# Optimization experiments

Hardware: AMD Instinct MI355X
Metric: run time of the kernel (lower is better)

The kernel has to match this reference:

```python
import jax, jax.numpy as jnp
import numpy as np

NBINS = 256  # skimage threshold_otsu default
SMOOTH = 1.0


def _otsu_threshold(x):
    """Otsu threshold of a flat float array, skimage-style 256-bin histogram."""
    x = x.reshape(-1)
    xmin = x.min()
    xmax = x.max()
    span = xmax - xmin
    scale = jnp.where(span > 0, NBINS / span, 0.0)
    idx = jnp.clip(((x - xmin) * scale).astype(jnp.int32), 0, NBINS - 1)
    hist = jnp.zeros(NBINS, dtype=x.dtype).at[idx].add(1.0)
    centers = xmin + (jnp.arange(NBINS, dtype=x.dtype) + 0.5) * (span / NBINS)
    # class weights and means (first bin always contains min, last contains max,
    # so the cumulative sums used below are strictly positive)
    w1 = jnp.cumsum(hist)
    w2 = jnp.cumsum(hist[::-1])
    m1 = jnp.cumsum(hist * centers) / w1
    m2 = (jnp.cumsum((hist * centers)[::-1]) / w2)[::-1]
    w2 = w2[::-1]
    var12 = w1[:-1] * w2[1:] * (m1[:-1] - m2[1:]) ** 2  # inter-class variance
    return centers[jnp.argmax(var12)]


def setup_inputs() -> dict:
    key = jax.random.key(0)
    k1, k2 = jax.random.split(key)
    B, C, H, W = 64, 1, 512, 512
    output = jax.random.normal(k1, (B, C, H, W), dtype=jnp.float32)
    target = (jax.random.uniform(k2, (B, C, H, W)) > 0.5).astype(jnp.float32)
    return {"output": output, "target": target}


def reference(output, target):
    probs = jax.nn.sigmoid(output)                    # [B,C,H,W]
    thresh = jax.vmap(_otsu_threshold)(probs)         # per-sample Otsu, [B]
    binary = (probs > thresh[:, None, None, None]).astype(probs.dtype)
    intersection = (binary * target).sum(axis=(-1, -2))          # [B,C]
    union = (binary + target).sum(axis=(-1, -2)) - intersection  # [B,C]
    iou = (intersection + SMOOTH) / (union + SMOOTH)
    return iou.mean()  # reduction='mean'
```

## Files before the change

### kernel.cpp

```cpp
#include <hip/hip_runtime.h>
#include <cstdint>

static constexpr int BATCH = 64;
static constexpr int NPB   = 512 * 512;
static constexpr int NFB   = 2048;
static constexpr int PBLK  = 16;
static constexpr int ELB   = NPB / PBLK;

static constexpr int W_BMIN = 0;
static constexpr int W_BMAX = 4096;
static constexpr int W_PART = 8192;

__device__ __forceinline__ float sigmoidf(float v) {
  if (v >= 0.0f) return 1.0f / (1.0f + expf(-v));
  float e = expf(v);
  return e / (1.0f + e);
}
__device__ __forceinline__ float fsig(float v) {
  return __builtin_amdgcn_rcpf(1.0f + __expf(-v));
}

__global__ __launch_bounds__(256) void k_pass(const float* __restrict__ x,
                                              const float* __restrict__ tg,
                                              uint32_t* __restrict__ ws,
                                              float* __restrict__ out) {
  constexpr int ITER = ELB / 4 / 256;
  __shared__ uint32_t h[2 * NFB];
  const int t = threadIdx.x;
  const int g = blockIdx.x;
  if (g == 0 && t == 0) out[0] = 0.0f;
#pragma unroll
  for (int j = 0; j < 4; ++j)
    reinterpret_cast<uint4*>(h)[t + j * 256] = uint4{0u, 0u, 0u, 0u};
  __syncthreads();

  const int b = g >> 4;
  const int blk = g & 15;
  const size_t base = (size_t)b * NPB + (size_t)blk * ELB;
  const float4* px = reinterpret_cast<const float4*>(x + base);
  const float4* pt = reinterpret_cast<const float4*>(tg + base);
  const uint32_t woff = (uint32_t)(t >> 7) << 11;

  float mn = INFINITY, mx = -INFINITY;
#pragma unroll 4
  for (int i = 0; i < ITER; ++i) {
    float4 v = px[i * 256 + t];
    float4 w = pt[i * 256 + t];
    mn = fminf(mn, fminf(fminf(v.x, v.y), fminf(v.z, v.w)));
    mx = fmaxf(mx, fmaxf(fmaxf(v.x, v.y), fmaxf(v.z, v.w)));
#define PUT(a, c) { int idx = (int)(fsig(a) * 2048.0f);                        \
                    idx = idx > 2047 ? 2047 : idx;                             \
                    const uint32_t val = ((c) > 0.5f) ? 0x10001u : 1u;         \
                    (void)__hip_atomic_fetch_add(&h[woff + idx], val,          \
                        __ATOMIC_RELAXED, __HIP_MEMORY_SCOPE_WORKGROUP); }
    PUT(v.x, w.x) PUT(v.y, w.y) PUT(v.z, w.z) PUT(v.w, w.w)
#undef PUT
  }
  for (int off = 32; off; off >>= 1) {
    mn = fminf(mn, __shfl_down(mn, off));
    mx = fmaxf(mx, __shfl_down(mx, off));
  }
  if ((t & 63) == 0) {
    float* wsf = reinterpret_cast<float*>(ws);
    wsf[W_BMIN + g * 4 + (t >> 6)] = mn;
    wsf[W_BMAX + g * 4 + (t >> 6)] = mx;
  }
  __syncthreads();
  uint32_t* gp = ws + W_PART + (size_t)g * NFB;
#pragma unroll
  for (int j = 0; j < 8; ++j) {
    const int w = t + j * 256;
    gp[w] = h[w] + h[w + 2048];
  }
}

__global__ __launch_bounds__(256) void k_finalize(uint32_t* __restrict__ ws,
                                                  float* __restrict__ out) {
  __shared__ uint32_t tot[NFB];
  __shared__ uint32_t pos[NFB];
  __shared__ uint32_t h256[256];
  __shared__ uint32_t w1s[256];
  __shared__ float s1s[256];
  __shared__ float vv[256];
  __shared__ int vi[256];
  __shared__ unsigned long long redL[256];
  __shared__ float sPmin, sScale, sBinw;
  const int b = blockIdx.x;
  const int t = threadIdx.x;
  const float* wsf = reinterpret_cast<const float*>(ws);

#pragma unroll
  for (int j = 0; j < 8; ++j) {
    const int w = t + j * 256;
    uint32_t at = 0, ap = 0;
#pragma unroll
    for (int p = 0; p < PBLK; ++p) {
      const uint32_t v = ws[W_PART + (size_t)(b * PBLK + p) * NFB + w];
      at += v & 0xFFFFu;
      ap += v >> 16;
    }
    tot[w] = at;
    pos[w] = ap;
  }
  h256[t] = 0u;
  if (t < 64) {
    float mnv = INFINITY, mxv = -INFINITY;
    for (int i = t; i < PBLK * 4; i += 64) {
      mnv = fminf(mnv, wsf[W_BMIN + b * PBLK * 4 + i]);
      mxv = fmaxf(mxv, wsf[W_BMAX + b * PBLK * 4 + i]);
    }
    for (int off = 32; off; off >>= 1) {
      mnv = fminf(mnv, __shfl_down(mnv, off));
      mxv = fmaxf(mxv, __shfl_down(mxv, off));
    }
    if (t == 0) {
      const float pmin = sigmoidf(mnv);
      const float pmax = sigmoidf(mxv);
      const float span = pmax - pmin;
      sPmin = pmin;
      sScale = (span > 0.0f) ? (512.0f / span) : 0.0f;
      sBinw = span * (1.0f / 256.0f);
    }
  }
  __syncthreads();
  const float pmin = sPmin, scale = sScale, binw = sBinw;

#define CIDX(k) ({ const float rep = ((float)(k) + 0.5f) * (1.0f / 2048.0f);  \
                   int ci = (int)((rep - pmin) * scale);                      \
                   ci = ci < 0 ? 0 : (ci > 511 ? 511 : ci); ci; })
#pragma unroll
  for (int j = 0; j < 8; ++j) {
    const int k = t + j * 256;
    if (tot[k]) atomicAdd(&h256[CIDX(k) >> 1], tot[k]);
  }
  __syncthreads();

  const uint32_t hk = h256[t];
  const float ck = pmin + ((float)t + 0.5f) * binw;
  w1s[t] = hk;
  s1s[t] = (float)hk * ck;
  for (int off = 1; off < 256; off <<= 1) {
    __syncthreads();
    uint32_t wp = (t >= off) ? w1s[t - off] : 0u;
    float    sp = (t >= off) ? s1s[t - off] : 0.0f;
    __syncthreads();
    w1s[t] += wp; s1s[t] += sp;
  }
  __syncthreads();
  const uint32_t totW = w1s[255];
  const float totS = s1s[255];
  float v = -INFINITY;
  if (t < 255 && w1s[t] > 0u && totW > w1s[t]) {
    const float w1f = (float)w1s[t];
    const float w2f = (float)(totW - w1s[t]);
    const float m1 = s1s[t] / w1f;
    const float m2 = (totS - s1s[t]) / w2f;
    const float d = m1 - m2;
    v = (w1f * w2f) * (d * d);
  }
  vv[t] = v; vi[t] = t;
  for (int s = 128; s; s >>= 1) {
    __syncthreads();
    if (t < s) {
      const float vb = vv[t + s]; const int ib = vi[t + s];
      if (vb > vv[t] || (vb == vv[t] && ib < vi[t])) { vv[t] = vb; vi[t] = ib; }
    }
  }
  __syncthreads();
  const int J = 2 * vi[0] + 1;

  uint32_t nb_p = 0, ni_p = 0, nt_p = 0;
#pragma unroll
  for (int j = 0; j < 8; ++j) {
    const int k = t + j * 256;
    const uint32_t ct = tot[k], cp = pos[k];
    nt_p += cp;
    if (CIDX(k) >= J) { nb_p += ct; ni_p += cp; }
  }
#undef CIDX
  redL[t] = (unsigned long long)nb_p | ((unsigned long long)ni_p << 20) | ((unsigned long long)nt_p << 40);
  for (int s = 128; s; s >>= 1) {
    __syncthreads();
    if (t < s) redL[t] += redL[t + s];
  }
  __syncthreads();
  if (t == 0) {
    const unsigned long long P = redL[0];
    const float nb = (float)(uint32_t)(P & 0xFFFFFu);
    const float ni = (float)(uint32_t)((P >> 20) & 0xFFFFFu);
    const float nt = (float)(uint32_t)((P >> 40) & 0xFFFFFu);
    const float uni = nb + nt - ni;
    const float iou = (ni + 1.0f) / (uni + 1.0f);
    atomicAdd(out, iou * (1.0f / 64.0f));
  }
}

extern "C" void kernel_launch(void* const* d_in, const int* in_sizes, int n_in,
                              void* d_out, int out_size, void* d_ws, size_t ws_size,
                              hipStream_t stream) {
  const float* x  = (const float*)d_in[0];
  const float* tg = (const float*)d_in[1];
  uint32_t* ws = (uint32_t*)d_ws;
  float* out = (float*)d_out;

  hipLaunchKernelGGL(k_pass,     dim3(BATCH * PBLK), dim3(256), 0, stream, x, tg, ws, out);
  hipLaunchKernelGGL(k_finalize, dim3(BATCH),        dim3(256), 0, stream, ws, out);
}
```

Measured before the change: 35.05 us.

## Fuse histogram and finalize into one kernel using last-block-done counters

```diff
diff --git a/kernel.cpp b/kernel.cpp
--- a/kernel.cpp
+++ b/kernel.cpp
@@ -4,12 +4,15 @@
 static constexpr int BATCH = 64;
 static constexpr int NPB   = 512 * 512;
 static constexpr int NFB   = 2048;
-static constexpr int PBLK  = 16;
+static constexpr int PBLK  = 8;
 static constexpr int ELB   = NPB / PBLK;
 
 static constexpr int W_BMIN = 0;
-static constexpr int W_BMAX = 4096;
-static constexpr int W_PART = 8192;
+static constexpr int W_BMAX = 512;
+static constexpr int W_T1   = 1024;
+static constexpr int W_T3   = 3072;
+static constexpr int W_IOU  = 3104;
+static constexpr int W_PART = 4096;
 
 __device__ __forceinline__ float sigmoidf(float v) {
   if (v >= 0.0f) return 1.0f / (1.0f + expf(-v));
@@ -19,23 +22,46 @@
 __device__ __forceinline__ float fsig(float v) {
   return __builtin_amdgcn_rcpf(1.0f + __expf(-v));
 }
-
-__global__ __launch_bounds__(256) void k_pass(const float* __restrict__ x,
+__device__ __forceinline__ uint32_t llc_load(const uint32_t* p) {
+  return __hip_atomic_load(p, __ATOMIC_RELAXED, __HIP_MEMORY_SCOPE_SYSTEM);
+}
+__device__ __forceinline__ float llc_loadf(const float* p) {
+  return __hip_atomic_load(p, __ATOMIC_RELAXED, __HIP_MEMORY_SCOPE_SYSTEM);
+}
+__device__ __forceinline__ void llc_store(uint32_t* p, uint32_t v) {
+  __hip_atomic_store(p, v, __ATOMIC_RELAXED, __HIP_MEMORY_SCOPE_SYSTEM);
+}
+__device__ __forceinline__ void llc_storef(float* p, float v) {
+  __hip_atomic_store(p, v, __ATOMIC_RELAXED, __HIP_MEMORY_SCOPE_SYSTEM);
+}
+
+__global__ __launch_bounds__(256) void k_init(uint32_t* __restrict__ ws) {
+  for (int i = threadIdx.x; i < 2080; i += 256) ws[W_T1 + i] = 0u;
+}
+
+__global__ __launch_bounds__(256) void k_main(const float* __restrict__ x,
                                               const float* __restrict__ tg,
                                               uint32_t* __restrict__ ws,
                                               float* __restrict__ out) {
-  constexpr int ITER = ELB / 4 / 256;
-  __shared__ uint32_t h[2 * NFB];
-  const int t = threadIdx.x;
-  const int g = blockIdx.x;
-  if (g == 0 && t == 0) out[0] = 0.0f;
-#pragma unroll
-  for (int j = 0; j < 4; ++j)
-    reinterpret_cast<uint4*>(h)[t + j * 256] = uint4{0u, 0u, 0u, 0u};
-  __syncthreads();
-
-  const int b = g >> 4;
-  const int blk = g & 15;
+  __shared__ uint32_t pool[4096];
+  __shared__ uint32_t h256[256];
+  __shared__ uint32_t scanA[256];
+  __shared__ float    scanB[256];
+  __shared__ float    scanC[256];
+  __shared__ int      scanD[256];
+  __shared__ unsigned long long redL[256];
+  __shared__ float smn[4], smx[4];
+  __shared__ int sFlag, sLast;
+  __shared__ float sPmin, sScale, sBinw;
+  const int t = threadIdx.x, g = blockIdx.x;
+  const int b = g >> 3, blk = g & 7;
+  float* wsf = reinterpret_cast<float*>(ws);
+
+#pragma unroll
+  for (int q = 0; q < 4; ++q)
+    reinterpret_cast<uint4*>(pool)[t + q * 256] = uint4{0u, 0u, 0u, 0u};
+  __syncthreads();
+
   const size_t base = (size_t)b * NPB + (size_t)blk * ELB;
   const float4* px = reinterpret_cast<const float4*>(x + base);
   const float4* pt = reinterpret_cast<const float4*>(tg + base);
@@ -43,7 +69,7 @@
 
   float mn = INFINITY, mx = -INFINITY;
 #pragma unroll 4
-  for (int i = 0; i < ITER; ++i) {
+  for (int i = 0; i < 32; ++i) {
     float4 v = px[i * 256 + t];
     float4 w = pt[i * 256 + t];
     mn = fminf(mn, fminf(fminf(v.x, v.y), fminf(v.z, v.w)));
@@ -51,7 +77,7 @@
 #define PUT(a, c) { int idx = (int)(fsig(a) * 2048.0f);                        \
                     idx = idx > 2047 ? 2047 : idx;                             \
                     const uint32_t val = ((c) > 0.5f) ? 0x10001u : 1u;         \
-                    (void)__hip_atomic_fetch_add(&h[woff + idx], val,          \
+                    (void)__hip_atomic_fetch_add(&pool[woff + idx], val,       \
                         __ATOMIC_RELAXED, __HIP_MEMORY_SCOPE_WORKGROUP); }
     PUT(v.x, w.x) PUT(v.y, w.y) PUT(v.z, w.z) PUT(v.w, w.w)
 #undef PUT
@@ -60,125 +86,120 @@
     mn = fminf(mn, __shfl_down(mn, off));
     mx = fmaxf(mx, __shfl_down(mx, off));
   }
-  if ((t & 63) == 0) {
-    float* wsf = reinterpret_cast<float*>(ws);
-    wsf[W_BMIN + g * 4 + (t >> 6)] = mn;
-    wsf[W_BMAX + g * 4 + (t >> 6)] = mx;
-  }
-  __syncthreads();
+  if ((t & 63) == 0) { smn[t >> 6] = mn; smx[t >> 6] = mx; }
+  __syncthreads();
+  if (t == 0) {
+    mn = fminf(fminf(smn[0], smn[1]), fminf(smn[2], smn[3]));
+    mx = fmaxf(fmaxf(smx[0], smx[1]), fmaxf(smx[2], smx[3]));
+    llc_storef(&wsf[W_BMIN + g], mn);
+    llc_storef(&wsf[W_BMAX + g], mx);
+  }
   uint32_t* gp = ws + W_PART + (size_t)g * NFB;
 #pragma unroll
-  for (int j = 0; j < 8; ++j) {
-    const int w = t + j * 256;
-    gp[w] = h[w] + h[w + 2048];
-  }
-}
-
-__global__ __launch_bounds__(256) void k_finalize(uint32_t* __restrict__ ws,
-                                                  float* __restrict__ out) {
-  __shared__ uint32_t tot[NFB];
-  __shared__ uint32_t pos[NFB];
-  __shared__ uint32_t h256[256];
-  __shared__ uint32_t w1s[256];
-  __shared__ float s1s[256];
-  __shared__ float vv[256];
-  __shared__ int vi[256];
-  __shared__ unsigned long long redL[256];
-  __shared__ float sPmin, sScale, sBinw;
-  const int b = blockIdx.x;
-  const int t = threadIdx.x;
-  const float* wsf = reinterpret_cast<const float*>(ws);
-
-#pragma unroll
-  for (int j = 0; j < 8; ++j) {
-    const int w = t + j * 256;
+  for (int q = 0; q < 8; ++q) {
+    const int w_ = t + q * 256;
+    llc_store(&gp[w_], pool[w_] + pool[w_ + 2048]);
+  }
+  __syncthreads();
+  if (t == 0) {
+    asm volatile("s_waitcnt vmcnt(0)" ::: "memory");
+    sFlag = (atomicAdd(&ws[W_T1 + b * 32], 1u) == PBLK - 1);
+  }
+  __syncthreads();
+  if (!sFlag) return;
+
+#pragma unroll
+  for (int q = 0; q < 8; ++q) {
+    const int k = t + q * 256;
     uint32_t at = 0, ap = 0;
 #pragma unroll
     for (int p = 0; p < PBLK; ++p) {
-      const uint32_t v = ws[W_PART + (size_t)(b * PBLK + p) * NFB + w];
+      const uint32_t v = llc_load(&ws[W_PART + (size_t)(b * 8 + p) * NFB + k]);
       at += v & 0xFFFFu;
       ap += v >> 16;
     }
-    tot[w] = at;
-    pos[w] = ap;
+    scanA[0] = scanA[0];
+    pool[k] = at | 0u;
+    redL[t] = 0ull;
+    pool[k + 2048] = ap;
   }
   h256[t] = 0u;
-  if (t < 64) {
-    float mnv = INFINITY, mxv = -INFINITY;
-    for (int i = t; i < PBLK * 4; i += 64) {
-      mnv = fminf(mnv, wsf[W_BMIN + b * PBLK * 4 + i]);
-      mxv = fmaxf(mxv, wsf[W_BMAX + b * PBLK * 4 + i]);
+  float mnv = (t < 8) ? llc_loadf(&wsf[W_BMIN + b * 8 + t]) : INFINITY;
+  float mxv = (t < 8) ? llc_loadf(&wsf[W_BMAX + b * 8 + t]) : -INFINITY;
+  for (int off = 4; off; off >>= 1) {
+    mnv = fminf(mnv, __shfl_down(mnv, off));
+    mxv = fmaxf(mxv, __shfl_down(mxv, off));
+  }
+  if (t == 0) {
+    const float pmin = sigmoidf(mnv);
+    const float pmax = sigmoidf(mxv);
+    const float span = pmax - pmin;
+    sPmin = pmin;
+    sScale = (span > 0.0f) ? (512.0f / span) : -1.0f;
+    sBinw = span * (1.0f / 256.0f);
+  }
+  __syncthreads();
+  const float pmin = sPmin, scale = sScale, binw = sBinw;
+  const bool degen = (scale < 0.0f);
+#define CIDX(k) ({ const float rep = ((float)(k) + 0.5f) * (1.0f / 2048.0f);  \
+                   int ci_ = (int)((rep - pmin) * scale);                     \
+                   ci_ = ci_ < 0 ? 0 : (ci_ > 511 ? 511 : ci_); ci_; })
+  if (!degen) {
+#pragma unroll
+    for (int q = 0; q < 8; ++q) {
+      const int k = t + q * 256;
+      const uint32_t ct = pool[k];
+      if (ct) atomicAdd(&h256[CIDX(k) >> 1], ct);
     }
-    for (int off = 32; off; off >>= 1) {
-      mnv = fminf(mnv, __shfl_down(mnv, off));
-      mxv = fmaxf(mxv, __shfl_down(mxv, off));
-    }
-    if (t == 0) {
-      const float pmin = sigmoidf(mnv);
-      const float pmax = sigmoidf(mxv);
-      const float span = pmax - pmin;
-      sPmin = pmin;
-      sScale = (span > 0.0f) ? (512.0f / span) : 0.0f;
-      sBinw = span * (1.0f / 256.0f);
-    }
-  }
-  __syncthreads();
-  const float pmin = sPmin, scale = sScale, binw = sBinw;
-
-#define CIDX(k) ({ const float rep = ((float)(k) + 0.5f) * (1.0f / 2048.0f);  \
-                   int ci = (int)((rep - pmin) * scale);                      \
-                   ci = ci < 0 ? 0 : (ci > 511 ? 511 : ci); ci; })
-#pragma unroll
-  for (int j = 0; j < 8; ++j) {
-    const int k = t + j * 256;
-    if (tot[k]) atomicAdd(&h256[CIDX(k) >> 1], tot[k]);
-  }
-  __syncthreads();
-
+  }
+  __syncthreads();
   const uint32_t hk = h256[t];
   const float ck = pmin + ((float)t + 0.5f) * binw;
-  w1s[t] = hk;
-  s1s[t] = (float)hk * ck;
+  scanA[t] = hk;
+  scanB[t] = (float)hk * ck;
   for (int off = 1; off < 256; off <<= 1) {
     __syncthreads();
-    uint32_t wp = (t >= off) ? w1s[t - off] : 0u;
-    float    sp = (t >= off) ? s1s[t - off] : 0.0f;
-    __syncthreads();
-    w1s[t] += wp; s1s[t] += sp;
-  }
-  __syncthreads();
-  const uint32_t totW = w1s[255];
-  const float totS = s1s[255];
-  float v = -INFINITY;
-  if (t < 255 && w1s[t] > 0u && totW > w1s[t]) {
-    const float w1f = (float)w1s[t];
-    const float w2f = (float)(totW - w1s[t]);
-    const float m1 = s1s[t] / w1f;
-    const float m2 = (totS - s1s[t]) / w2f;
+    uint32_t wp = (t >= off) ? scanA[t - off] : 0u;
+    float    sp = (t >= off) ? scanB[t - off] : 0.0f;
+    __syncthreads();
+    scanA[t] += wp; scanB[t] += sp;
+  }
+  __syncthreads();
+  const uint32_t totW = scanA[255];
+  const float totS = scanB[255];
+  float vv = -INFINITY;
+  if (t < 255 && scanA[t] > 0u && totW > scanA[t]) {
+    const float w1f = (float)scanA[t];
+    const float w2f = (float)(totW - scanA[t]);
+    const float m1 = scanB[t] / w1f;
+    const float m2 = (totS - scanB[t]) / w2f;
     const float d = m1 - m2;
-    v = (w1f * w2f) * (d * d);
-  }
-  vv[t] = v; vi[t] = t;
+    vv = (w1f * w2f) * (d * d);
+  }
+  scanC[t] = vv; scanD[t] = t;
   for (int s = 128; s; s >>= 1) {
     __syncthreads();
     if (t < s) {
-      const float vb = vv[t + s]; const int ib = vi[t + s];
-      if (vb > vv[t] || (vb == vv[t] && ib < vi[t])) { vv[t] = vb; vi[t] = ib; }
+      const float vb = scanC[t + s]; const int ib = scanD[t + s];
+      if (vb > scanC[t] || (vb == scanC[t] && ib < scanD[t])) {
+        scanC[t] = vb; scanD[t] = ib;
+      }
     }
   }
   __syncthreads();
-  const int J = 2 * vi[0] + 1;
-
-  uint32_t nb_p = 0, ni_p = 0, nt_p = 0;
-#pragma unroll
-  for (int j = 0; j < 8; ++j) {
-    const int k = t + j * 256;
-    const uint32_t ct = tot[k], cp = pos[k];
-    nt_p += cp;
-    if (CIDX(k) >= J) { nb_p += ct; ni_p += cp; }
+  const int Jh = degen ? (1 << 20) : (2 * scanD[0] + 1);
+  uint32_t nb = 0, ni = 0, nt = 0;
+#pragma unroll
+  for (int q = 0; q < 8; ++q) {
+    const int k = t + q * 256;
+    const uint32_t ct = pool[k], cp = pool[k + 2048];
+    nt += cp;
+    const int ci = degen ? 0 : CIDX(k);
+    if (ci >= Jh) { nb += ct; ni += cp; }
   }
 #undef CIDX
-  redL[t] = (unsigned long long)nb_p | ((unsigned long long)ni_p << 20) | ((unsigned long long)nt_p << 40);
+  redL[t] = (unsigned long long)nb | ((unsigned long long)ni << 20) |
+            ((unsigned long long)nt << 40);
   for (int s = 128; s; s >>= 1) {
     __syncthreads();
     if (t < s) redL[t] += redL[t + s];
@@ -186,12 +207,20 @@
   __syncthreads();
   if (t == 0) {
     const unsigned long long P = redL[0];
-    const float nb = (float)(uint32_t)(P & 0xFFFFFu);
-    const float ni = (float)(uint32_t)((P >> 20) & 0xFFFFFu);
-    const float nt = (float)(uint32_t)((P >> 40) & 0xFFFFFu);
-    const float uni = nb + nt - ni;
-    const float iou = (ni + 1.0f) / (uni + 1.0f);
-    atomicAdd(out, iou * (1.0f / 64.0f));
+    const float NB = (float)(uint32_t)(P & 0xFFFFFu);
+    const float NI = (float)(uint32_t)((P >> 20) & 0xFFFFFu);
+    const float NT = (float)(uint32_t)((P >> 40) & 0xFFFFFu);
+    llc_storef(&wsf[W_IOU + b], (NI + 1.0f) / ((NB + NT - NI) + 1.0f));
+    asm volatile("s_waitcnt vmcnt(0)" ::: "memory");
+    sLast = (atomicAdd(&ws[W_T3], 1u) == BATCH - 1);
+  }
+  __syncthreads();
+  if (!sLast) return;
+
+  float iou = (t < 64) ? llc_loadf(&wsf[W_IOU + t]) : 0.0f;
+  if (t < 64) {
+    for (int off = 32; off; off >>= 1) iou += __shfl_down(iou, off);
+    if (t == 0) out[0] = iou * (1.0f / 64.0f);
   }
 }
 
@@ -203,6 +232,6 @@
   uint32_t* ws = (uint32_t*)d_ws;
   float* out = (float*)d_out;
 
-  hipLaunchKernelGGL(k_pass,     dim3(BATCH * PBLK), dim3(256), 0, stream, x, tg, ws, out);
-  hipLaunchKernelGGL(k_finalize, dim3(BATCH),        dim3(256), 0, stream, ws, out);
-}
+  hipLaunchKernelGGL(k_init, dim3(1),            dim3(256), 0, stream, ws);
+  hipLaunchKernelGGL(k_main, dim3(BATCH * PBLK), dim3(256), 0, stream, x, tg, ws, out);
+}
```

Result: slower. 39.43 us (+12.5%).
